# Optimization experiments

Hardware: AMD Instinct MI355X
Metric: run time of the kernel (lower is better)

The kernel has to match this reference:

```python
import math
import jax, jax.numpy as jnp
import numpy as np

L, H, D, FF, V, S = 12, 12, 768, 3072, 32000, 1024
HD = D // H
EPS = 1e-5
B, T = 2, 1024


def layernorm(x, w, b):
    mu = jnp.mean(x, axis=-1, keepdims=True)
    var = jnp.mean(jnp.square(x - mu), axis=-1, keepdims=True)
    return (x - mu) * jax.lax.rsqrt(var + EPS) * w + b


def setup_inputs() -> dict:
    key = jax.random.key(0)
    ks = jax.random.split(key, 12)
    std = 0.02
    std_res = 0.02 / math.sqrt(2 * L)  # out_proj / down_proj scaled init
    return {
        "input_ids": jax.random.randint(ks[0], (B, T), 0, V),
        "tok_emb": jax.random.normal(ks[1], (V, D), jnp.float32) * std,
        "pos_emb": jax.random.normal(ks[2], (S, D), jnp.float32) * std,
        "ln1_w": jnp.ones((L, D), jnp.float32),
        "ln1_b": jnp.zeros((L, D), jnp.float32),
        "qkv_w": jax.random.normal(ks[3], (L, 3 * D, D), jnp.float32) * std,
        "out_w": jax.random.normal(ks[4], (L, D, D), jnp.float32) * std_res,
        "ln2_w": jnp.ones((L, D), jnp.float32),
        "ln2_b": jnp.zeros((L, D), jnp.float32),
        "up_w": jax.random.normal(ks[5], (L, FF, D), jnp.float32) * std,
        "down_w": jax.random.normal(ks[6], (L, D, FF), jnp.float32) * std_res,
        "lnf_w": jnp.ones((D,), jnp.float32),
        "lnf_b": jnp.zeros((D,), jnp.float32),
    }


def reference(input_ids, tok_emb, pos_emb, ln1_w, ln1_b, qkv_w, out_w,
              ln2_w, ln2_b, up_w, down_w, lnf_w, lnf_b):
    b, t = input_ids.shape
    x = tok_emb[input_ids] + pos_emb[:t]  # (B,T,D); dropout = eval no-op
    causal = jnp.tril(jnp.ones((t, t), bool))  # (T,T)
    scale = 1.0 / math.sqrt(HD)

    def block(x, p):
        l1w, l1b, qkvw, ow, l2w, l2b, uw, dw = p
        h = layernorm(x, l1w, l1b)
        qkv = h @ qkvw.T  # (B,T,3D)
        q, k, v = jnp.split(qkv, 3, axis=-1)
        q = q.reshape(b, t, H, HD)
        k = k.reshape(b, t, H, HD)
        v = v.reshape(b, t, H, HD)
        scores = jnp.einsum('bihd,bjhd->bhij', q, k) * scale
        scores = jnp.where(causal, scores, -jnp.inf)
        probs = jax.nn.softmax(scores, axis=-1)  # attn_dropout = eval no-op
        o = jnp.einsum('bhij,bjhd->bihd', probs, v).reshape(b, t, D)
        x = x + o @ ow.T
        h2 = layernorm(x, l2w, l2b)
        x = x + jax.nn.gelu(h2 @ uw.T, approximate=False) @ dw.T
        return x, None

    x, _ = jax.lax.scan(block, x, (ln1_w, ln1_b, qkv_w, out_w, ln2_w, ln2_b, up_w, down_w))
    x = layernorm(x, lnf_w, lnf_b)
    logits = x @ tok_emb.T  # tied lm_head
    return logits
```

## Files before the change

### kernel.cpp

```cpp
#include <hip/hip_runtime.h>
#include <hip/hip_bf16.h>
#include <math.h>

#define L_  12
#define H_  12
#define D_  768
#define FF_ 3072
#define V_  32000
#define T_  1024
#define B_  2
#define BT_ (B_*T_)

typedef unsigned short ushort_t;
typedef unsigned int   uint_t;
typedef __bf16 bf16x8 __attribute__((ext_vector_type(8)));
typedef float  f32x4  __attribute__((ext_vector_type(4)));

__device__ __forceinline__ uint_t f2bf1(float f) {
    uint_t u = __builtin_bit_cast(uint_t, f);
    return (u + 0x7FFFu + ((u >> 16) & 1u)) >> 16;
}
__device__ __forceinline__ uint_t f2bf2(float lo, float hi) {
    return f2bf1(lo) | (f2bf1(hi) << 16);
}

__device__ __forceinline__ void gl_lds16(const ushort_t* g, ushort_t* l) {
    __builtin_amdgcn_global_load_lds(
        (const __attribute__((address_space(1))) uint_t*)g,
        (__attribute__((address_space(3))) uint_t*)l, 16, 0, 0);
}

__global__ __launch_bounds__(256) void cast_bf16(const float* __restrict__ in,
                                                 ushort_t* __restrict__ out, int n8)
{
    for (int i = blockIdx.x * 256 + threadIdx.x; i < n8; i += gridDim.x * 256) {
        const float4* p = (const float4*)(in + (size_t)i * 8);
        float4 a = p[0], b = p[1];
        *(uint4*)(out + (size_t)i * 8) =
            make_uint4(f2bf2(a.x,a.y), f2bf2(a.z,a.w), f2bf2(b.x,b.y), f2bf2(b.z,b.w));
    }
}

__global__ __launch_bounds__(256) void cast_layer(const float* __restrict__ q,
    const float* __restrict__ o, const float* __restrict__ u, const float* __restrict__ d,
    ushort_t* __restrict__ out)
{
    const int N0 = 3*D_*D_/8, N1 = N0 + D_*D_/8, N2 = N1 + FF_*D_/8, N3 = N2 + D_*FF_/8;
    for (int i = blockIdx.x * 256 + threadIdx.x; i < N3; i += gridDim.x * 256) {
        const float* src;
        if      (i < N0) src = q + (size_t)i * 8;
        else if (i < N1) src = o + (size_t)(i - N0) * 8;
        else if (i < N2) src = u + (size_t)(i - N1) * 8;
        else             src = d + (size_t)(i - N2) * 8;
        const float4* p = (const float4*)src;
        float4 a = p[0], b = p[1];
        *(uint4*)(out + (size_t)i * 8) =
            make_uint4(f2bf2(a.x,a.y), f2bf2(a.z,a.w), f2bf2(b.x,b.y), f2bf2(b.z,b.w));
    }
}

#define EPI_F32   0
#define EPI_BF16  1
#define EPI_GELU  2
#define EPI_PART  3

template <int EPI, int BM, int KS>
__global__ __launch_bounds__(256) void gemm_bt(
    const ushort_t* __restrict__ A, const ushort_t* __restrict__ W,
    const float* R, void* Cv, int N, int K, int Kc)
{
    constexpr int MI = BM / 32;
    constexpr int AH = BM * 64;
    constexpr int BH = 128 * 64;
    __shared__ ushort_t As[2 * AH];
    __shared__ ushort_t Bs[2 * BH];

    const int tid  = threadIdx.x;
    const int w    = tid >> 6;
    const int lane = tid & 63;

    const int nwg = gridDim.x;
    int swz = (blockIdx.x & 7) * (nwg >> 3) + (blockIdx.x >> 3);
    constexpr int MT = 2048 / BM;
    const int mt = swz & (MT - 1);
    int rest     = swz / MT;
    const int ks = rest & (KS - 1);
    const int nt = rest / KS;
    const int m0 = mt * BM, n0 = nt * 128;
    const int kb = ks * Kc;

    const int srow = lane >> 3;
    const int scol = ((lane & 7) ^ srow) * 8;
    const ushort_t* gA = A + (size_t)(m0 + w * (BM / 4) + srow) * K + scol;
    const ushort_t* gW = W + (size_t)(n0 + w * 32 + srow) * K + scol;
    const size_t row8 = (size_t)8 * K;

    const int lr = lane & 15;
    const int lg = lane >> 4;
    const int wm = (w >> 1) * (BM / 2);
    const int wn = (w & 1) * 64;

    f32x4 acc[MI][4] = {};

    auto stage = [&](int buf, int k0) {
        ushort_t* lA = As + buf * AH + w * (BM / 4) * 64;
        ushort_t* lB = Bs + buf * BH + w * 2048;
        #pragma unroll
        for (int i = 0; i < BM / 32; ++i)
            gl_lds16(gA + k0 + i * row8, lA + i * 512);
        #pragma unroll
        for (int i = 0; i < 4; ++i)
            gl_lds16(gW + k0 + i * row8, lB + i * 512);
    };

    stage(0, kb);
    __syncthreads();
    int cur = 0;
    for (int k0 = kb; k0 < kb + Kc; k0 += 64) {
        if (k0 + 64 < kb + Kc) stage(cur ^ 1, k0 + 64);
        const ushort_t* Ab = As + cur * AH;
        const ushort_t* Bb = Bs + cur * BH;
        __builtin_amdgcn_s_setprio(1);
        #pragma unroll
        for (int kk = 0; kk < 2; ++kk) {
            bf16x8 av[MI], bv[4];
            #pragma unroll
            for (int i = 0; i < MI; ++i) {
                int rr = wm + i * 16 + lr;
                int ch = (lg + 4 * kk) ^ (rr & 7);
                av[i] = *(const bf16x8*)&Ab[rr * 64 + ch * 8];
            }
            #pragma unroll
            for (int j = 0; j < 4; ++j) {
                int rr = wn + j * 16 + lr;
                int ch = (lg + 4 * kk) ^ (rr & 7);
                bv[j] = *(const bf16x8*)&Bb[rr * 64 + ch * 8];
            }
            #pragma unroll
            for (int i = 0; i < MI; ++i)
                #pragma unroll
                for (int j = 0; j < 4; ++j)
                    acc[i][j] = __builtin_amdgcn_mfma_f32_16x16x32_bf16(av[i], bv[j], acc[i][j], 0, 0, 0);
        }
        __builtin_amdgcn_s_setprio(0);
        __syncthreads();
        cur ^= 1;
    }

    float*    Cf = (float*)Cv;
    ushort_t* Cb = (ushort_t*)Cv;
    float*    Pp = (EPI == EPI_PART) ? (ks ? const_cast<float*>(R) : (float*)Cv) : nullptr;
    const int rbase = lg * 4;
    #pragma unroll
    for (int i = 0; i < MI; ++i) {
        #pragma unroll
        for (int j = 0; j < 4; ++j) {
            #pragma unroll
            for (int r = 0; r < 4; ++r) {
                int row = m0 + wm + i * 16 + rbase + r;
                int col = n0 + wn + j * 16 + lr;
                size_t idx = (size_t)row * N + col;
                float v = acc[i][j][r];
                if (EPI == EPI_F32)  Cf[idx] = v;
                if (EPI == EPI_BF16) Cb[idx] = (ushort_t)f2bf1(v);
                if (EPI == EPI_GELU) Cb[idx] = (ushort_t)f2bf1(0.5f * v * (1.0f + erff(v * 0.70710678118654752f)));
                if (EPI == EPI_PART) Pp[idx] = v;
            }
        }
    }
}

__global__ __launch_bounds__(256) void vprep(const ushort_t* __restrict__ qkv,
                                             ushort_t* __restrict__ vt)
{
    __shared__ ushort_t Vs[64][72];
    const int blk   = blockIdx.x;
    const int ttile = blk & 15;
    const int bh    = blk >> 4;
    const int b     = bh / H_;
    const int h     = bh % H_;
    const int tid   = threadIdx.x;
    const int t0    = ttile * 64;
    {
        const int tr = tid >> 2;
        const int dc = (tid & 3) * 16;
        const uint4* src = (const uint4*)(qkv + (size_t)(b * T_ + t0 + tr) * 2304 + 1536 + h * 64 + dc);
        uint4 v0 = src[0], v1 = src[1];
        *(uint4*)&Vs[tr][dc]     = v0;
        *(uint4*)&Vs[tr][dc + 8] = v1;
    }
    __syncthreads();
    {
        const int d  = tid >> 2;
        const int jc = (tid & 3) * 16;
        uint_t w[8];
        #pragma unroll
        for (int i = 0; i < 8; ++i)
            w[i] = (uint_t)Vs[jc + 2*i][d] | ((uint_t)Vs[jc + 2*i + 1][d] << 16);
        uint4* dst = (uint4*)(vt + ((size_t)bh * 64 + d) * T_ + t0 + jc);
        dst[0] = make_uint4(w[0], w[1], w[2], w[3]);
        dst[1] = make_uint4(w[4], w[5], w[6], w[7]);
    }
}

__global__ __launch_bounds__(64) void attn_mfma(const ushort_t* __restrict__ qkv,
    const ushort_t* __restrict__ vt, ushort_t* __restrict__ o)
{
    __shared__ ushort_t Ps[16 * 136];

    int swz = (blockIdx.x & 7) * 192 + (blockIdx.x >> 3);
    const int bh  = swz >> 6;
    const int qtl = 63 - (swz & 63);
    const int b   = bh / H_;
    const int h   = bh % H_;
    const int lane = threadIdx.x;
    const int l15  = lane & 15;
    const int lg   = lane >> 4;
    const int qbase = qtl * 16;
    const int qlast = qbase + 15;

    const ushort_t* qp = qkv + ((size_t)(b * T_) + qbase + l15) * 2304 + h * 64 + lg * 8;
    bf16x8 qf0 = *(const bf16x8*)qp;
    bf16x8 qf1 = *(const bf16x8*)(qp + 32);

    f32x4 od[4] = {};
    float mr[4] = {-INFINITY, -INFINITY, -INFINITY, -INFINITY};
    float lr[4] = {0.f, 0.f, 0.f, 0.f};

    const ushort_t* kbase = qkv + (size_t)(b * T_) * 2304 + 768 + h * 64;
    const ushort_t* vbase = vt + (size_t)bh * 64 * T_;
    const float SC = 0.18033688011112042f;

    for (int j0 = 0; j0 <= qlast; j0 += 128) {
        f32x4 s[8];
        __builtin_amdgcn_s_setprio(1);
        #pragma unroll
        for (int n = 0; n < 8; ++n) {
            if (j0 + 16 * n <= qlast) {
                const ushort_t* kr = kbase + (size_t)(j0 + 16 * n + l15) * 2304 + lg * 8;
                bf16x8 kf0 = *(const bf16x8*)kr;
                bf16x8 kf1 = *(const bf16x8*)(kr + 32);
                f32x4 a = {};
                a = __builtin_amdgcn_mfma_f32_16x16x32_bf16(qf0, kf0, a, 0, 0, 0);
                a = __builtin_amdgcn_mfma_f32_16x16x32_bf16(qf1, kf1, a, 0, 0, 0);
                s[n] = a;
            } else {
                s[n] = f32x4{-INFINITY, -INFINITY, -INFINITY, -INFINITY};
            }
        }
        __builtin_amdgcn_s_setprio(0);

        #pragma unroll
        for (int n = 0; n < 8; ++n) {
            #pragma unroll
            for (int r = 0; r < 4; ++r) {
                float v = s[n][r] * SC;
                int jg = j0 + 16 * n + l15;
                int qg = qbase + lg * 4 + r;
                if (jg > qg) v = -INFINITY;
                s[n][r] = v;
            }
        }

        float al[4];
        #pragma unroll
        for (int r = 0; r < 4; ++r) {
            float tm = fmaxf(fmaxf(fmaxf(s[0][r], s[1][r]), fmaxf(s[2][r], s[3][r])),
                             fmaxf(fmaxf(s[4][r], s[5][r]), fmaxf(s[6][r], s[7][r])));
            tm = fmaxf(tm, __shfl_xor(tm, 1, 64));
            tm = fmaxf(tm, __shfl_xor(tm, 2, 64));
            tm = fmaxf(tm, __shfl_xor(tm, 4, 64));
            tm = fmaxf(tm, __shfl_xor(tm, 8, 64));
            float mn = fmaxf(mr[r], tm);
            al[r] = exp2f(mr[r] - mn);
            mr[r] = mn;
        }
        #pragma unroll
        for (int n = 0; n < 8; ++n)
            #pragma unroll
            for (int r = 0; r < 4; ++r)
                s[n][r] = exp2f(s[n][r] - mr[r]);
        #pragma unroll
        for (int r = 0; r < 4; ++r) {
            float ps = (s[0][r] + s[1][r]) + (s[2][r] + s[3][r]);
            ps += (s[4][r] + s[5][r]) + (s[6][r] + s[7][r]);
            ps += __shfl_xor(ps, 1, 64);
            ps += __shfl_xor(ps, 2, 64);
            ps += __shfl_xor(ps, 4, 64);
            ps += __shfl_xor(ps, 8, 64);
            lr[r] = lr[r] * al[r] + ps;
        }
        #pragma unroll
        for (int n = 0; n < 4; ++n)
            #pragma unroll
            for (int r = 0; r < 4; ++r)
                od[n][r] *= al[r];

        #pragma unroll
        for (int n = 0; n < 8; ++n)
            #pragma unroll
            for (int r = 0; r < 4; ++r)
                Ps[(lg * 4 + r) * 136 + 16 * n + l15] = (ushort_t)f2bf1(s[n][r]);

        __builtin_amdgcn_s_setprio(1);
        #pragma unroll
        for (int kc = 0; kc < 4; ++kc) {
            if (j0 + kc * 32 <= qlast) {
                bf16x8 pa = *(const bf16x8*)&Ps[l15 * 136 + kc * 32 + lg * 8];
                #pragma unroll
                for (int nn = 0; nn < 4; ++nn) {
                    bf16x8 vf = *(const bf16x8*)&vbase[(size_t)(16 * nn + l15) * T_ + j0 + kc * 32 + lg * 8];
                    od[nn] = __builtin_amdgcn_mfma_f32_16x16x32_bf16(pa, vf, od[nn], 0, 0, 0);
                }
            }
        }
        __builtin_amdgcn_s_setprio(0);
    }

    #pragma unroll
    for (int r = 0; r < 4; ++r) {
        float inv = 1.0f / lr[r];
        int row = qbase + lg * 4 + r;
        ushort_t* op = o + ((size_t)(b * T_ + row)) * 768 + h * 64 + l15;
        #pragma unroll
        for (int nn = 0; nn < 4; ++nn)
            op[16 * nn] = (ushort_t)f2bf1(od[nn][r] * inv);
    }
}

__global__ __launch_bounds__(256) void ln_kernel(const float* __restrict__ x,
    const float* __restrict__ w, const float* __restrict__ bia, ushort_t* __restrict__ out)
{
    const int row = blockIdx.x;
    const int tid = threadIdx.x;
    const float* xr = x + (size_t)row * 768;
    float v0 = xr[tid], v1 = xr[tid + 256], v2 = xr[tid + 512];
    float s  = v0 + v1 + v2;
    float s2 = v0 * v0 + v1 * v1 + v2 * v2;
    #pragma unroll
    for (int off = 32; off > 0; off >>= 1) {
        s  += __shfl_down(s,  off, 64);
        s2 += __shfl_down(s2, off, 64);
    }
    __shared__ float sh[8];
    const int wave = tid >> 6;
    if ((tid & 63) == 0) { sh[wave] = s; sh[4 + wave] = s2; }
    __syncthreads();
    float S  = sh[0] + sh[1] + sh[2] + sh[3];
    float S2 = sh[4] + sh[5] + sh[6] + sh[7];
    float mean = S * (1.f / 768.f);
    float var  = S2 * (1.f / 768.f) - mean * mean;
    float inv  = rsqrtf(var + 1e-5f);
    ushort_t* orow = out + (size_t)row * 768;
    orow[tid]       = (ushort_t)f2bf1((v0 - mean) * inv * w[tid]       + bia[tid]);
    orow[tid + 256] = (ushort_t)f2bf1((v1 - mean) * inv * w[tid + 256] + bia[tid + 256]);
    orow[tid + 512] = (ushort_t)f2bf1((v2 - mean) * inv * w[tid + 512] + bia[tid + 512]);
}

__global__ __launch_bounds__(256) void ln_red(float* __restrict__ x,
    const float* __restrict__ P0, const float* __restrict__ P1,
    const float* __restrict__ w, const float* __restrict__ bia, ushort_t* __restrict__ out)
{
    const int row = blockIdx.x;
    const int tid = threadIdx.x;
    const size_t base = (size_t)row * 768;
    float v0 = x[base + tid]       + P0[base + tid]       + P1[base + tid];
    float v1 = x[base + tid + 256] + P0[base + tid + 256] + P1[base + tid + 256];
    float v2 = x[base + tid + 512] + P0[base + tid + 512] + P1[base + tid + 512];
    x[base + tid]       = v0;
    x[base + tid + 256] = v1;
    x[base + tid + 512] = v2;
    float s  = v0 + v1 + v2;
    float s2 = v0 * v0 + v1 * v1 + v2 * v2;
    #pragma unroll
    for (int off = 32; off > 0; off >>= 1) {
        s  += __shfl_down(s,  off, 64);
        s2 += __shfl_down(s2, off, 64);
    }
    __shared__ float sh[8];
    const int wave = tid >> 6;
    if ((tid & 63) == 0) { sh[wave] = s; sh[4 + wave] = s2; }
    __syncthreads();
    float S  = sh[0] + sh[1] + sh[2] + sh[3];
    float S2 = sh[4] + sh[5] + sh[6] + sh[7];
    float mean = S * (1.f / 768.f);
    float var  = S2 * (1.f / 768.f) - mean * mean;
    float inv  = rsqrtf(var + 1e-5f);
    ushort_t* orow = out + base;
    orow[tid]       = (ushort_t)f2bf1((v0 - mean) * inv * w[tid]       + bia[tid]);
    orow[tid + 256] = (ushort_t)f2bf1((v1 - mean) * inv * w[tid + 256] + bia[tid + 256]);
    orow[tid + 512] = (ushort_t)f2bf1((v2 - mean) * inv * w[tid + 512] + bia[tid + 512]);
}

__global__ __launch_bounds__(256) void embed_kernel(const int* __restrict__ ids,
    const float* __restrict__ tok, const float* __restrict__ pos, float* __restrict__ x)
{
    const int bt = blockIdx.x;
    const int t  = bt % T_;
    const int id = ids[bt];
    const int tid = threadIdx.x;
    const float* tr = tok + (size_t)id * 768;
    const float* pr = pos + (size_t)t * 768;
    float* xr = x + (size_t)bt * 768;
    xr[tid]       = tr[tid]       + pr[tid];
    xr[tid + 256] = tr[tid + 256] + pr[tid + 256];
    xr[tid + 512] = tr[tid + 512] + pr[tid + 512];
}

extern "C" void kernel_launch(void* const* d_in, const int* in_sizes, int n_in,
                              void* d_out, int out_size, void* d_ws, size_t ws_size,
                              hipStream_t stream)
{
    const int*   ids   = (const int*)  d_in[0];
    const float* tok   = (const float*)d_in[1];
    const float* pos   = (const float*)d_in[2];
    const float* ln1w  = (const float*)d_in[3];
    const float* ln1b  = (const float*)d_in[4];
    const float* qkvw  = (const float*)d_in[5];
    const float* outw  = (const float*)d_in[6];
    const float* ln2w  = (const float*)d_in[7];
    const float* ln2b  = (const float*)d_in[8];
    const float* upw   = (const float*)d_in[9];
    const float* downw = (const float*)d_in[10];
    const float* lnfw  = (const float*)d_in[11];
    const float* lnfb  = (const float*)d_in[12];
    float* out = (float*)d_out;

    char* ws = (char*)d_ws;
    ushort_t* h    = (ushort_t*)ws;
    float*    x    = (float*)   (ws + 3145728);
    ushort_t* qkv  = (ushort_t*)(ws + 9437184);
    ushort_t* o    = qkv  + (size_t)BT_ * 3 * D_;
    ushort_t* vt   = o    + (size_t)BT_ * D_;
    ushort_t* ffh  = vt   + (size_t)B_ * H_ * 64 * T_;
    ushort_t* layerW = ffh + (size_t)BT_ * FF_;
    ushort_t* tokW = (ushort_t*)(ws + 3145728);

    float* Pa     = (float*)(ws + 9437184);
    float* Pb_out = (float*)ffh;
    float* Pb_dwn = (float*)(ws + 18874368);

    ushort_t* qkvwB  = layerW;
    ushort_t* outwB  = qkvwB + (size_t)3 * D_ * D_;
    ushort_t* upwB   = outwB + (size_t)D_ * D_;
    ushort_t* downwB = upwB  + (size_t)FF_ * D_;

    embed_kernel<<<BT_, 256, 0, stream>>>(ids, tok, pos, x);

    for (int l = 0; l < L_; ++l) {
        cast_layer<<<1024, 256, 0, stream>>>(
            qkvw  + (size_t)l * 3 * D_ * D_,
            outw  + (size_t)l * D_ * D_,
            upw   + (size_t)l * FF_ * D_,
            downw + (size_t)l * D_ * FF_, layerW);

        if (l == 0)
            ln_kernel<<<BT_, 256, 0, stream>>>(x, ln1w, ln1b, h);
        else
            ln_red<<<BT_, 256, 0, stream>>>(x, Pa, Pb_dwn, ln1w + l * D_, ln1b + l * D_, h);

        gemm_bt<EPI_BF16, 128, 1><<<16 * (3 * D_ / 128), 256, 0, stream>>>(
            h, qkvwB, nullptr, qkv, 3 * D_, D_, D_);

        vprep<<<B_ * H_ * (T_ / 64), 256, 0, stream>>>(qkv, vt);
        attn_mfma<<<B_ * H_ * (T_ / 16), 64, 0, stream>>>(qkv, vt, o);

        gemm_bt<EPI_PART, 64, 2><<<32 * (D_ / 128) * 2, 256, 0, stream>>>(
            o, outwB, Pb_out, Pa, D_, D_, D_ / 2);

        ln_red<<<BT_, 256, 0, stream>>>(x, Pa, Pb_out, ln2w + l * D_, ln2b + l * D_, h);

        gemm_bt<EPI_GELU, 128, 1><<<16 * (FF_ / 128), 256, 0, stream>>>(
            h, upwB, nullptr, ffh, FF_, D_, D_);

        gemm_bt<EPI_PART, 64, 2><<<32 * (D_ / 128) * 2, 256, 0, stream>>>(
            ffh, downwB, Pb_dwn, Pa, D_, FF_, FF_ / 2);
    }

    ln_red<<<BT_, 256, 0, stream>>>(x, Pa, Pb_dwn, lnfw, lnfb, h);
    cast_bf16<<<2048, 256, 0, stream>>>(tok, tokW, V_ * D_ / 8);

    for (int c = 0; c < 5; ++c) {
        gemm_bt<EPI_F32, 128, 1><<<16 * 50, 256, 0, stream>>>(
            h, tokW + (size_t)c * 6400 * D_, nullptr, out + (size_t)c * 6400, V_, D_, D_);
    }
}
```

Measured before the change: 2.052 ms.

## Widen attention to 32-query tiles, hoist weight casts, merge LM-head GEMM

```diff
diff --git a/kernel.cpp b/kernel.cpp
--- a/kernel.cpp
+++ b/kernel.cpp
@@ -35,24 +35,6 @@
 {
     for (int i = blockIdx.x * 256 + threadIdx.x; i < n8; i += gridDim.x * 256) {
         const float4* p = (const float4*)(in + (size_t)i * 8);
-        float4 a = p[0], b = p[1];
-        *(uint4*)(out + (size_t)i * 8) =
-            make_uint4(f2bf2(a.x,a.y), f2bf2(a.z,a.w), f2bf2(b.x,b.y), f2bf2(b.z,b.w));
-    }
-}
-
-__global__ __launch_bounds__(256) void cast_layer(const float* __restrict__ q,
-    const float* __restrict__ o, const float* __restrict__ u, const float* __restrict__ d,
-    ushort_t* __restrict__ out)
-{
-    const int N0 = 3*D_*D_/8, N1 = N0 + D_*D_/8, N2 = N1 + FF_*D_/8, N3 = N2 + D_*FF_/8;
-    for (int i = blockIdx.x * 256 + threadIdx.x; i < N3; i += gridDim.x * 256) {
-        const float* src;
-        if      (i < N0) src = q + (size_t)i * 8;
-        else if (i < N1) src = o + (size_t)(i - N0) * 8;
-        else if (i < N2) src = u + (size_t)(i - N1) * 8;
-        else             src = d + (size_t)(i - N2) * 8;
-        const float4* p = (const float4*)src;
         float4 a = p[0], b = p[1];
         *(uint4*)(out + (size_t)i * 8) =
             make_uint4(f2bf2(a.x,a.y), f2bf2(a.z,a.w), f2bf2(b.x,b.y), f2bf2(b.z,b.w));
@@ -206,33 +188,40 @@
 __global__ __launch_bounds__(64) void attn_mfma(const ushort_t* __restrict__ qkv,
     const ushort_t* __restrict__ vt, ushort_t* __restrict__ o)
 {
-    __shared__ ushort_t Ps[16 * 136];
-
-    int swz = (blockIdx.x & 7) * 192 + (blockIdx.x >> 3);
-    const int bh  = swz >> 6;
-    const int qtl = 63 - (swz & 63);
+    __shared__ ushort_t Ps[32 * 136];
+
+    int swz = (blockIdx.x & 7) * 96 + (blockIdx.x >> 3);
+    const int bh  = swz >> 5;
+    const int qtl = 31 - (swz & 31);
     const int b   = bh / H_;
     const int h   = bh % H_;
     const int lane = threadIdx.x;
     const int l15  = lane & 15;
     const int lg   = lane >> 4;
-    const int qbase = qtl * 16;
-    const int qlast = qbase + 15;
-
-    const ushort_t* qp = qkv + ((size_t)(b * T_) + qbase + l15) * 2304 + h * 64 + lg * 8;
-    bf16x8 qf0 = *(const bf16x8*)qp;
-    bf16x8 qf1 = *(const bf16x8*)(qp + 32);
-
-    f32x4 od[4] = {};
-    float mr[4] = {-INFINITY, -INFINITY, -INFINITY, -INFINITY};
-    float lr[4] = {0.f, 0.f, 0.f, 0.f};
+    const int qbase = qtl * 32;
+    const int qlast = qbase + 31;
+
+    bf16x8 qf[2][2];
+    #pragma unroll
+    for (int g = 0; g < 2; ++g) {
+        const ushort_t* qp = qkv + ((size_t)(b * T_) + qbase + g * 16 + l15) * 2304 + h * 64 + lg * 8;
+        qf[g][0] = *(const bf16x8*)qp;
+        qf[g][1] = *(const bf16x8*)(qp + 32);
+    }
+
+    f32x4 od[2][4] = {};
+    float mr[2][4], lr_[2][4];
+    #pragma unroll
+    for (int g = 0; g < 2; ++g)
+        #pragma unroll
+        for (int r = 0; r < 4; ++r) { mr[g][r] = -INFINITY; lr_[g][r] = 0.f; }
 
     const ushort_t* kbase = qkv + (size_t)(b * T_) * 2304 + 768 + h * 64;
     const ushort_t* vbase = vt + (size_t)bh * 64 * T_;
     const float SC = 0.18033688011112042f;
 
     for (int j0 = 0; j0 <= qlast; j0 += 128) {
-        f32x4 s[8];
+        f32x4 s[2][8];
         __builtin_amdgcn_s_setprio(1);
         #pragma unroll
         for (int n = 0; n < 8; ++n) {
@@ -240,77 +229,87 @@
                 const ushort_t* kr = kbase + (size_t)(j0 + 16 * n + l15) * 2304 + lg * 8;
                 bf16x8 kf0 = *(const bf16x8*)kr;
                 bf16x8 kf1 = *(const bf16x8*)(kr + 32);
-                f32x4 a = {};
-                a = __builtin_amdgcn_mfma_f32_16x16x32_bf16(qf0, kf0, a, 0, 0, 0);
-                a = __builtin_amdgcn_mfma_f32_16x16x32_bf16(qf1, kf1, a, 0, 0, 0);
-                s[n] = a;
+                #pragma unroll
+                for (int g = 0; g < 2; ++g) {
+                    f32x4 a = {};
+                    a = __builtin_amdgcn_mfma_f32_16x16x32_bf16(qf[g][0], kf0, a, 0, 0, 0);
+                    a = __builtin_amdgcn_mfma_f32_16x16x32_bf16(qf[g][1], kf1, a, 0, 0, 0);
+                    s[g][n] = a;
+                }
             } else {
-                s[n] = f32x4{-INFINITY, -INFINITY, -INFINITY, -INFINITY};
+                s[0][n] = f32x4{-INFINITY, -INFINITY, -INFINITY, -INFINITY};
+                s[1][n] = f32x4{-INFINITY, -INFINITY, -INFINITY, -INFINITY};
             }
         }
         __builtin_amdgcn_s_setprio(0);
 
         #pragma unroll
-        for (int n = 0; n < 8; ++n) {
+        for (int g = 0; g < 2; ++g)
+            #pragma unroll
+            for (int n = 0; n < 8; ++n)
+                #pragma unroll
+                for (int r = 0; r < 4; ++r) {
+                    float v = s[g][n][r] * SC;
+                    int jg = j0 + 16 * n + l15;
+                    int qg = qbase + g * 16 + lg * 4 + r;
+                    if (jg > qg) v = -INFINITY;
+                    s[g][n][r] = v;
+                }
+
+        #pragma unroll
+        for (int g = 0; g < 2; ++g) {
+            float al[4];
             #pragma unroll
             for (int r = 0; r < 4; ++r) {
-                float v = s[n][r] * SC;
-                int jg = j0 + 16 * n + l15;
-                int qg = qbase + lg * 4 + r;
-                if (jg > qg) v = -INFINITY;
-                s[n][r] = v;
-            }
-        }
-
-        float al[4];
-        #pragma unroll
-        for (int r = 0; r < 4; ++r) {
-            float tm = fmaxf(fmaxf(fmaxf(s[0][r], s[1][r]), fmaxf(s[2][r], s[3][r])),
-                             fmaxf(fmaxf(s[4][r], s[5][r]), fmaxf(s[6][r], s[7][r])));
-            tm = fmaxf(tm, __shfl_xor(tm, 1, 64));
-            tm = fmaxf(tm, __shfl_xor(tm, 2, 64));
-            tm = fmaxf(tm, __shfl_xor(tm, 4, 64));
-            tm = fmaxf(tm, __shfl_xor(tm, 8, 64));
-            float mn = fmaxf(mr[r], tm);
-            al[r] = exp2f(mr[r] - mn);
-            mr[r] = mn;
-        }
-        #pragma unroll
-        for (int n = 0; n < 8; ++n)
-            #pragma unroll
-            for (int r = 0; r < 4; ++r)
-                s[n][r] = exp2f(s[n][r] - mr[r]);
-        #pragma unroll
-        for (int r = 0; r < 4; ++r) {
-            float ps = (s[0][r] + s[1][r]) + (s[2][r] + s[3][r]);
-            ps += (s[4][r] + s[5][r]) + (s[6][r] + s[7][r]);
-            ps += __shfl_xor(ps, 1, 64);
-            ps += __shfl_xor(ps, 2, 64);
-            ps += __shfl_xor(ps, 4, 64);
-            ps += __shfl_xor(ps, 8, 64);
-            lr[r] = lr[r] * al[r] + ps;
-        }
-        #pragma unroll
-        for (int n = 0; n < 4; ++n)
-            #pragma unroll
-            for (int r = 0; r < 4; ++r)
-                od[n][r] *= al[r];
-
-        #pragma unroll
-        for (int n = 0; n < 8; ++n)
-            #pragma unroll
-            for (int r = 0; r < 4; ++r)
-                Ps[(lg * 4 + r) * 136 + 16 * n + l15] = (ushort_t)f2bf1(s[n][r]);
+                float tm = fmaxf(fmaxf(fmaxf(s[g][0][r], s[g][1][r]), fmaxf(s[g][2][r], s[g][3][r])),
+                                 fmaxf(fmaxf(s[g][4][r], s[g][5][r]), fmaxf(s[g][6][r], s[g][7][r])));
+                tm = fmaxf(tm, __shfl_xor(tm, 1, 64));
+                tm = fmaxf(tm, __shfl_xor(tm, 2, 64));
+                tm = fmaxf(tm, __shfl_xor(tm, 4, 64));
+                tm = fmaxf(tm, __shfl_xor(tm, 8, 64));
+                float mn = fmaxf(mr[g][r], tm);
+                al[r] = exp2f(mr[g][r] - mn);
+                mr[g][r] = mn;
+            }
+            #pragma unroll
+            for (int n = 0; n < 8; ++n)
+                #pragma unroll
+                for (int r = 0; r < 4; ++r)
+                    s[g][n][r] = exp2f(s[g][n][r] - mr[g][r]);
+            #pragma unroll
+            for (int r = 0; r < 4; ++r) {
+                float ps = (s[g][0][r] + s[g][1][r]) + (s[g][2][r] + s[g][3][r]);
+                ps += (s[g][4][r] + s[g][5][r]) + (s[g][6][r] + s[g][7][r]);
+                ps += __shfl_xor(ps, 1, 64);
+                ps += __shfl_xor(ps, 2, 64);
+                ps += __shfl_xor(ps, 4, 64);
+                ps += __shfl_xor(ps, 8, 64);
+                lr_[g][r] = lr_[g][r] * al[r] + ps;
+            }
+            #pragma unroll
+            for (int n = 0; n < 4; ++n)
+                #pragma unroll
+                for (int r = 0; r < 4; ++r)
+                    od[g][n][r] *= al[r];
+
+            #pragma unroll
+            for (int n = 0; n < 8; ++n)
+                #pragma unroll
+                for (int r = 0; r < 4; ++r)
+                    Ps[(g * 16 + lg * 4 + r) * 136 + 16 * n + l15] = (ushort_t)f2bf1(s[g][n][r]);
+        }
 
         __builtin_amdgcn_s_setprio(1);
         #pragma unroll
         for (int kc = 0; kc < 4; ++kc) {
             if (j0 + kc * 32 <= qlast) {
-                bf16x8 pa = *(const bf16x8*)&Ps[l15 * 136 + kc * 32 + lg * 8];
+                bf16x8 paA = *(const bf16x8*)&Ps[l15 * 136 + kc * 32 + lg * 8];
+                bf16x8 paB = *(const bf16x8*)&Ps[(16 + l15) * 136 + kc * 32 + lg * 8];
                 #pragma unroll
                 for (int nn = 0; nn < 4; ++nn) {
                     bf16x8 vf = *(const bf16x8*)&vbase[(size_t)(16 * nn + l15) * T_ + j0 + kc * 32 + lg * 8];
-                    od[nn] = __builtin_amdgcn_mfma_f32_16x16x32_bf16(pa, vf, od[nn], 0, 0, 0);
+                    od[0][nn] = __builtin_amdgcn_mfma_f32_16x16x32_bf16(paA, vf, od[0][nn], 0, 0, 0);
+                    od[1][nn] = __builtin_amdgcn_mfma_f32_16x16x32_bf16(paB, vf, od[1][nn], 0, 0, 0);
                 }
             }
         }
@@ -318,14 +317,16 @@
     }
 
     #pragma unroll
-    for (int r = 0; r < 4; ++r) {
-        float inv = 1.0f / lr[r];
-        int row = qbase + lg * 4 + r;
-        ushort_t* op = o + ((size_t)(b * T_ + row)) * 768 + h * 64 + l15;
-        #pragma unroll
-        for (int nn = 0; nn < 4; ++nn)
-            op[16 * nn] = (ushort_t)f2bf1(od[nn][r] * inv);
-    }
+    for (int g = 0; g < 2; ++g)
+        #pragma unroll
+        for (int r = 0; r < 4; ++r) {
+            float inv = 1.0f / lr_[g][r];
+            int row = qbase + g * 16 + lg * 4 + r;
+            ushort_t* op = o + ((size_t)(b * T_ + row)) * 768 + h * 64 + l15;
+            #pragma unroll
+            for (int nn = 0; nn < 4; ++nn)
+                op[16 * nn] = (ushort_t)f2bf1(od[g][nn][r] * inv);
+        }
 }
 
 __global__ __launch_bounds__(256) void ln_kernel(const float* __restrict__ x,
@@ -433,55 +434,48 @@
     ushort_t* o    = qkv  + (size_t)BT_ * 3 * D_;
     ushort_t* vt   = o    + (size_t)BT_ * D_;
     ushort_t* ffh  = vt   + (size_t)B_ * H_ * 64 * T_;
-    ushort_t* layerW = ffh + (size_t)BT_ * FF_;
-    ushort_t* tokW = (ushort_t*)(ws + 3145728);
-
-    float* Pa     = (float*)(ws + 9437184);
-    float* Pb_out = (float*)ffh;
-    float* Pb_dwn = (float*)(ws + 18874368);
-
-    ushort_t* qkvwB  = layerW;
-    ushort_t* outwB  = qkvwB + (size_t)3 * D_ * D_;
-    ushort_t* upwB   = outwB + (size_t)D_ * D_;
-    ushort_t* downwB = upwB  + (size_t)FF_ * D_;
+    float*    Pa   = (float*)(ws + 37748736);
+    float*    Pb   = (float*)(ws + 44040192);
+    ushort_t* qkvwB  = (ushort_t*)(ws + 50331648);
+    ushort_t* outwB  = qkvwB  + (size_t)L_ * 3 * D_ * D_;
+    ushort_t* upwB   = outwB  + (size_t)L_ * D_ * D_;
+    ushort_t* downwB = upwB   + (size_t)L_ * FF_ * D_;
+    ushort_t* tokW   = downwB + (size_t)L_ * D_ * FF_;
+
+    cast_bf16<<<2048, 256, 0, stream>>>(qkvw,  qkvwB,  L_ * 3 * D_ * D_ / 8);
+    cast_bf16<<<2048, 256, 0, stream>>>(outw,  outwB,  L_ * D_ * D_ / 8);
+    cast_bf16<<<2048, 256, 0, stream>>>(upw,   upwB,   L_ * FF_ * D_ / 8);
+    cast_bf16<<<2048, 256, 0, stream>>>(downw, downwB, L_ * D_ * FF_ / 8);
+    cast_bf16<<<2048, 256, 0, stream>>>(tok,   tokW,   V_ * D_ / 8);
 
     embed_kernel<<<BT_, 256, 0, stream>>>(ids, tok, pos, x);
 
     for (int l = 0; l < L_; ++l) {
-        cast_layer<<<1024, 256, 0, stream>>>(
-            qkvw  + (size_t)l * 3 * D_ * D_,
-            outw  + (size_t)l * D_ * D_,
-            upw   + (size_t)l * FF_ * D_,
-            downw + (size_t)l * D_ * FF_, layerW);
-
         if (l == 0)
             ln_kernel<<<BT_, 256, 0, stream>>>(x, ln1w, ln1b, h);
         else
-            ln_red<<<BT_, 256, 0, stream>>>(x, Pa, Pb_dwn, ln1w + l * D_, ln1b + l * D_, h);
+            ln_red<<<BT_, 256, 0, stream>>>(x, Pa, Pb, ln1w + l * D_, ln1b + l * D_, h);
 
         gemm_bt<EPI_BF16, 128, 1><<<16 * (3 * D_ / 128), 256, 0, stream>>>(
-            h, qkvwB, nullptr, qkv, 3 * D_, D_, D_);
+            h, qkvwB + (size_t)l * 3 * D_ * D_, nullptr, qkv, 3 * D_, D_, D_);
 
         vprep<<<B_ * H_ * (T_ / 64), 256, 0, stream>>>(qkv, vt);
-        attn_mfma<<<B_ * H_ * (T_ / 16), 64, 0, stream>>>(qkv, vt, o);
+        attn_mfma<<<B_ * H_ * (T_ / 32), 64, 0, stream>>>(qkv, vt, o);
 
         gemm_bt<EPI_PART, 64, 2><<<32 * (D_ / 128) * 2, 256, 0, stream>>>(
-            o, outwB, Pb_out, Pa, D_, D_, D_ / 2);
-
-        ln_red<<<BT_, 256, 0, stream>>>(x, Pa, Pb_out, ln2w + l * D_, ln2b + l * D_, h);
+            o, outwB + (size_t)l * D_ * D_, Pb, Pa, D_, D_, D_ / 2);
+
+        ln_red<<<BT_, 256, 0, stream>>>(x, Pa, Pb, ln2w + l * D_, ln2b + l * D_, h);
 
         gemm_bt<EPI_GELU, 128, 1><<<16 * (FF_ / 128), 256, 0, stream>>>(
-            h, upwB, nullptr, ffh, FF_, D_, D_);
+            h, upwB + (size_t)l * FF_ * D_, nullptr, ffh, FF_, D_, D_);
 
         gemm_bt<EPI_PART, 64, 2><<<32 * (D_ / 128) * 2, 256, 0, stream>>>(
-            ffh, downwB, Pb_dwn, Pa, D_, FF_, FF_ / 2);
-    }
-
-    ln_red<<<BT_, 256, 0, stream>>>(x, Pa, Pb_dwn, lnfw, lnfb, h);
-    cast_bf16<<<2048, 256, 0, stream>>>(tok, tokW, V_ * D_ / 8);
-
-    for (int c = 0; c < 5; ++c) {
-        gemm_bt<EPI_F32, 128, 1><<<16 * 50, 256, 0, stream>>>(
-            h, tokW + (size_t)c * 6400 * D_, nullptr, out + (size_t)c * 6400, V_, D_, D_);
-    }
-}
+            ffh, downwB + (size_t)l * D_ * FF_, Pb, Pa, D_, FF_, FF_ / 2);
+    }
+
+    ln_red<<<BT_, 256, 0, stream>>>(x, Pa, Pb, lnfw, lnfb, h);
+
+    gemm_bt<EPI_F32, 128, 1><<<16 * (V_ / 128), 256, 0, stream>>>(
+        h, tokW, nullptr, out, V_, D_, D_);
+}
```

After: 2.338 ms. 1.14x slower.

## Cast all layer weights upfront, halve GEMM K-tile, launch single lm_head GEMM

Applied to the files above, without the earlier changes.

```diff
diff --git a/kernel.cpp b/kernel.cpp
--- a/kernel.cpp
+++ b/kernel.cpp
@@ -41,24 +41,6 @@
     }
 }
 
-__global__ __launch_bounds__(256) void cast_layer(const float* __restrict__ q,
-    const float* __restrict__ o, const float* __restrict__ u, const float* __restrict__ d,
-    ushort_t* __restrict__ out)
-{
-    const int N0 = 3*D_*D_/8, N1 = N0 + D_*D_/8, N2 = N1 + FF_*D_/8, N3 = N2 + D_*FF_/8;
-    for (int i = blockIdx.x * 256 + threadIdx.x; i < N3; i += gridDim.x * 256) {
-        const float* src;
-        if      (i < N0) src = q + (size_t)i * 8;
-        else if (i < N1) src = o + (size_t)(i - N0) * 8;
-        else if (i < N2) src = u + (size_t)(i - N1) * 8;
-        else             src = d + (size_t)(i - N2) * 8;
-        const float4* p = (const float4*)src;
-        float4 a = p[0], b = p[1];
-        *(uint4*)(out + (size_t)i * 8) =
-            make_uint4(f2bf2(a.x,a.y), f2bf2(a.z,a.w), f2bf2(b.x,b.y), f2bf2(b.z,b.w));
-    }
-}
-
 #define EPI_F32   0
 #define EPI_BF16  1
 #define EPI_GELU  2
@@ -70,8 +52,8 @@
     const float* R, void* Cv, int N, int K, int Kc)
 {
     constexpr int MI = BM / 32;
-    constexpr int AH = BM * 64;
-    constexpr int BH = 128 * 64;
+    constexpr int AH = BM * 32;
+    constexpr int BH = 128 * 32;
     __shared__ ushort_t As[2 * AH];
     __shared__ ushort_t Bs[2 * BH];
 
@@ -89,11 +71,11 @@
     const int m0 = mt * BM, n0 = nt * 128;
     const int kb = ks * Kc;
 
-    const int srow = lane >> 3;
-    const int scol = ((lane & 7) ^ srow) * 8;
+    const int srow = lane >> 2;
+    const int scol = ((lane & 3) ^ ((srow >> 1) & 3)) * 8;
     const ushort_t* gA = A + (size_t)(m0 + w * (BM / 4) + srow) * K + scol;
     const ushort_t* gW = W + (size_t)(n0 + w * 32 + srow) * K + scol;
-    const size_t row8 = (size_t)8 * K;
+    const size_t row16 = (size_t)16 * K;
 
     const int lr = lane & 15;
     const int lg = lane >> 4;
@@ -103,38 +85,37 @@
     f32x4 acc[MI][4] = {};
 
     auto stage = [&](int buf, int k0) {
-        ushort_t* lA = As + buf * AH + w * (BM / 4) * 64;
-        ushort_t* lB = Bs + buf * BH + w * 2048;
-        #pragma unroll
-        for (int i = 0; i < BM / 32; ++i)
-            gl_lds16(gA + k0 + i * row8, lA + i * 512);
-        #pragma unroll
-        for (int i = 0; i < 4; ++i)
-            gl_lds16(gW + k0 + i * row8, lB + i * 512);
+        ushort_t* lA = As + buf * AH + w * (BM / 4) * 32;
+        ushort_t* lB = Bs + buf * BH + w * 1024;
+        #pragma unroll
+        for (int i = 0; i < BM / 64; ++i)
+            gl_lds16(gA + k0 + i * row16, lA + i * 512);
+        #pragma unroll
+        for (int i = 0; i < 2; ++i)
+            gl_lds16(gW + k0 + i * row16, lB + i * 512);
     };
 
     stage(0, kb);
     __syncthreads();
     int cur = 0;
-    for (int k0 = kb; k0 < kb + Kc; k0 += 64) {
-        if (k0 + 64 < kb + Kc) stage(cur ^ 1, k0 + 64);
+    for (int k0 = kb; k0 < kb + Kc; k0 += 32) {
+        if (k0 + 32 < kb + Kc) stage(cur ^ 1, k0 + 32);
         const ushort_t* Ab = As + cur * AH;
         const ushort_t* Bb = Bs + cur * BH;
         __builtin_amdgcn_s_setprio(1);
-        #pragma unroll
-        for (int kk = 0; kk < 2; ++kk) {
+        {
             bf16x8 av[MI], bv[4];
             #pragma unroll
             for (int i = 0; i < MI; ++i) {
                 int rr = wm + i * 16 + lr;
-                int ch = (lg + 4 * kk) ^ (rr & 7);
-                av[i] = *(const bf16x8*)&Ab[rr * 64 + ch * 8];
+                int ch = lg ^ ((rr >> 1) & 3);
+                av[i] = *(const bf16x8*)&Ab[rr * 32 + ch * 8];
             }
             #pragma unroll
             for (int j = 0; j < 4; ++j) {
                 int rr = wn + j * 16 + lr;
-                int ch = (lg + 4 * kk) ^ (rr & 7);
-                bv[j] = *(const bf16x8*)&Bb[rr * 64 + ch * 8];
+                int ch = lg ^ ((rr >> 1) & 3);
+                bv[j] = *(const bf16x8*)&Bb[rr * 32 + ch * 8];
             }
             #pragma unroll
             for (int i = 0; i < MI; ++i)
@@ -433,55 +414,48 @@
     ushort_t* o    = qkv  + (size_t)BT_ * 3 * D_;
     ushort_t* vt   = o    + (size_t)BT_ * D_;
     ushort_t* ffh  = vt   + (size_t)B_ * H_ * 64 * T_;
-    ushort_t* layerW = ffh + (size_t)BT_ * FF_;
-    ushort_t* tokW = (ushort_t*)(ws + 3145728);
-
-    float* Pa     = (float*)(ws + 9437184);
-    float* Pb_out = (float*)ffh;
-    float* Pb_dwn = (float*)(ws + 18874368);
-
-    ushort_t* qkvwB  = layerW;
-    ushort_t* outwB  = qkvwB + (size_t)3 * D_ * D_;
-    ushort_t* upwB   = outwB + (size_t)D_ * D_;
-    ushort_t* downwB = upwB  + (size_t)FF_ * D_;
+    float*    Pa   = (float*)(ws + 37748736);
+    float*    Pb   = (float*)(ws + 44040192);
+    ushort_t* qkvwB  = (ushort_t*)(ws + 50331648);
+    ushort_t* outwB  = qkvwB  + (size_t)L_ * 3 * D_ * D_;
+    ushort_t* upwB   = outwB  + (size_t)L_ * D_ * D_;
+    ushort_t* downwB = upwB   + (size_t)L_ * FF_ * D_;
+    ushort_t* tokW   = downwB + (size_t)L_ * D_ * FF_;
+
+    cast_bf16<<<2048, 256, 0, stream>>>(qkvw,  qkvwB,  L_ * 3 * D_ * D_ / 8);
+    cast_bf16<<<2048, 256, 0, stream>>>(outw,  outwB,  L_ * D_ * D_ / 8);
+    cast_bf16<<<2048, 256, 0, stream>>>(upw,   upwB,   L_ * FF_ * D_ / 8);
+    cast_bf16<<<2048, 256, 0, stream>>>(downw, downwB, L_ * D_ * FF_ / 8);
 
     embed_kernel<<<BT_, 256, 0, stream>>>(ids, tok, pos, x);
 
     for (int l = 0; l < L_; ++l) {
-        cast_layer<<<1024, 256, 0, stream>>>(
-            qkvw  + (size_t)l * 3 * D_ * D_,
-            outw  + (size_t)l * D_ * D_,
-            upw   + (size_t)l * FF_ * D_,
-            downw + (size_t)l * D_ * FF_, layerW);
-
         if (l == 0)
             ln_kernel<<<BT_, 256, 0, stream>>>(x, ln1w, ln1b, h);
         else
-            ln_red<<<BT_, 256, 0, stream>>>(x, Pa, Pb_dwn, ln1w + l * D_, ln1b + l * D_, h);
+            ln_red<<<BT_, 256, 0, stream>>>(x, Pa, Pb, ln1w + l * D_, ln1b + l * D_, h);
 
         gemm_bt<EPI_BF16, 128, 1><<<16 * (3 * D_ / 128), 256, 0, stream>>>(
-            h, qkvwB, nullptr, qkv, 3 * D_, D_, D_);
+            h, qkvwB + (size_t)l * 3 * D_ * D_, nullptr, qkv, 3 * D_, D_, D_);
 
         vprep<<<B_ * H_ * (T_ / 64), 256, 0, stream>>>(qkv, vt);
         attn_mfma<<<B_ * H_ * (T_ / 16), 64, 0, stream>>>(qkv, vt, o);
 
         gemm_bt<EPI_PART, 64, 2><<<32 * (D_ / 128) * 2, 256, 0, stream>>>(
-            o, outwB, Pb_out, Pa, D_, D_, D_ / 2);
-
-        ln_red<<<BT_, 256, 0, stream>>>(x, Pa, Pb_out, ln2w + l * D_, ln2b + l * D_, h);
+            o, outwB + (size_t)l * D_ * D_, Pb, Pa, D_, D_, D_ / 2);
+
+        ln_red<<<BT_, 256, 0, stream>>>(x, Pa, Pb, ln2w + l * D_, ln2b + l * D_, h);
 
         gemm_bt<EPI_GELU, 128, 1><<<16 * (FF_ / 128), 256, 0, stream>>>(
-            h, upwB, nullptr, ffh, FF_, D_, D_);
+            h, upwB + (size_t)l * FF_ * D_, nullptr, ffh, FF_, D_, D_);
 
         gemm_bt<EPI_PART, 64, 2><<<32 * (D_ / 128) * 2, 256, 0, stream>>>(
-            ffh, downwB, Pb_dwn, Pa, D_, FF_, FF_ / 2);
-    }
-
-    ln_red<<<BT_, 256, 0, stream>>>(x, Pa, Pb_dwn, lnfw, lnfb, h);
+            ffh, downwB + (size_t)l * D_ * FF_, Pb, Pa, D_, FF_, FF_ / 2);
+    }
+
+    ln_red<<<BT_, 256, 0, stream>>>(x, Pa, Pb, lnfw, lnfb, h);
+
     cast_bf16<<<2048, 256, 0, stream>>>(tok, tokW, V_ * D_ / 8);
-
-    for (int c = 0; c < 5; ++c) {
-        gemm_bt<EPI_F32, 128, 1><<<16 * 50, 256, 0, stream>>>(
-            h, tokW + (size_t)c * 6400 * D_, nullptr, out + (size_t)c * 6400, V_, D_, D_);
-    }
-}
+    gemm_bt<EPI_F32, 128, 1><<<16 * (V_ / 128), 256, 0, stream>>>(
+        h, tokW, nullptr, out, V_, D_, D_);
+}
```

New measurement: 2.234 ms. 8.8% more time.
